# Optimization experiments

Hardware: AMD Instinct MI355X
Metric: run time of the kernel (lower is better)

The kernel has to match this reference:

```python
import jax, jax.numpy as jnp
import numpy as np
import math

D_MODEL = 512
H = 8
DK = D_MODEL // H  # 64
DFF = 2048
EPS = 1e-5


def layernorm(x, g, b):
    mu = jnp.mean(x, axis=-1, keepdims=True)
    var = jnp.mean((x - mu) ** 2, axis=-1, keepdims=True)
    return (x - mu) * jax.lax.rsqrt(var + EPS) * g + b


def gelu(x):
    return jax.nn.gelu(x, approximate=False)  # torch nn.GELU default (erf)


def feedforward(x, W1, b1, lng, lnb, W2, b2):
    x1 = jnp.einsum('btd,df->btf', x, W1) + b1
    x1 = gelu(layernorm(x1, lng, lnb))
    return jnp.einsum('btf,fd->btd', x1, W2) + b2


def setup_inputs() -> dict:
    key = jax.random.key(0)
    ks = iter(jax.random.split(key, 32))
    s = 0.02
    d = {}
    d['x'] = jax.random.normal(next(ks), (4, 2048, D_MODEL), jnp.float32)
    # per-head QKV projections, stacked over heads: [H, d_model, dk]
    d['Wq'] = jax.random.normal(next(ks), (H, D_MODEL, DK), jnp.float32) * s
    d['bq'] = jnp.zeros((H, DK), jnp.float32)
    d['Wk'] = jax.random.normal(next(ks), (H, D_MODEL, DK), jnp.float32) * s
    d['bk'] = jnp.zeros((H, DK), jnp.float32)
    d['Wv'] = jax.random.normal(next(ks), (H, D_MODEL, DK), jnp.float32) * s
    d['bv'] = jnp.zeros((H, DK), jnp.float32)
    d['Wo'] = jax.random.normal(next(ks), (D_MODEL, D_MODEL), jnp.float32) * s
    d['bo'] = jnp.zeros((D_MODEL,), jnp.float32)
    d['ln1_g'] = jnp.ones((D_MODEL,), jnp.float32)
    d['ln1_b'] = jnp.zeros((D_MODEL,), jnp.float32)
    # main FFN
    d['ff_W1'] = jax.random.normal(next(ks), (D_MODEL, DFF), jnp.float32) * s
    d['ff_b1'] = jnp.zeros((DFF,), jnp.float32)
    d['ff_lng'] = jnp.ones((DFF,), jnp.float32)
    d['ff_lnb'] = jnp.zeros((DFF,), jnp.float32)
    d['ff_W2'] = jax.random.normal(next(ks), (DFF, D_MODEL), jnp.float32) * s
    d['ff_b2'] = jnp.zeros((D_MODEL,), jnp.float32)
    d['ln2_g'] = jnp.ones((D_MODEL,), jnp.float32)
    d['ln2_b'] = jnp.zeros((D_MODEL,), jnp.float32)
    d['alphaA'] = jnp.zeros((1,), jnp.float32) + 0.1
    d['alphaB'] = jnp.zeros((1,), jnp.float32) + 0.1
    d['p1'] = jnp.asarray(0.1, jnp.float32)
    # sub1 FFN
    d['s1_W1'] = jax.random.normal(next(ks), (D_MODEL, DFF), jnp.float32) * s
    d['s1_b1'] = jnp.zeros((DFF,), jnp.float32)
    d['s1_lng'] = jnp.ones((DFF,), jnp.float32)
    d['s1_lnb'] = jnp.zeros((DFF,), jnp.float32)
    d['s1_W2'] = jax.random.normal(next(ks), (DFF, D_MODEL), jnp.float32) * s
    d['s1_b2'] = jnp.zeros((D_MODEL,), jnp.float32)
    d['lnsub1_g'] = jnp.ones((D_MODEL,), jnp.float32)
    d['lnsub1_b'] = jnp.zeros((D_MODEL,), jnp.float32)
    d['p2'] = jnp.asarray(0.1, jnp.float32)
    d['sub2_W'] = jax.random.normal(next(ks), (D_MODEL, D_MODEL), jnp.float32) * s
    d['sub2_b'] = jnp.zeros((D_MODEL,), jnp.float32)
    d['lnsub2_g'] = jnp.ones((D_MODEL,), jnp.float32)
    d['lnsub2_b'] = jnp.zeros((D_MODEL,), jnp.float32)
    return d


def reference(x, Wq, bq, Wk, bk, Wv, bv, Wo, bo, ln1_g, ln1_b,
              ff_W1, ff_b1, ff_lng, ff_lnb, ff_W2, ff_b2, ln2_g, ln2_b,
              alphaA, alphaB, p1, s1_W1, s1_b1, s1_lng, s1_lnb, s1_W2, s1_b2,
              lnsub1_g, lnsub1_b, p2, sub2_W, sub2_b, lnsub2_g, lnsub2_b):
    # --- multi-head attention (q = k = v = x) ---
    q = jnp.einsum('btd,hdk->bhtk', x, Wq) + bq[:, None, :]
    k = jnp.einsum('btd,hdk->bhtk', x, Wk) + bk[:, None, :]
    v = jnp.einsum('btd,hdk->bhtk', x, Wv) + bv[:, None, :]
    scores = jnp.einsum('bhtk,bhsk->bhts', q, k) / math.sqrt(DK)
    probs = jax.nn.softmax(scores, axis=-1)
    heads = jnp.einsum('bhts,bhsv->bhtv', probs, v)           # [B,H,T,dv]
    B, _, T, _ = heads.shape
    cat = jnp.transpose(heads, (0, 2, 1, 3)).reshape(B, T, H * DK)
    attn = jnp.einsum('btd,de->bte', cat, Wo) + bo
    # --- residual stack ---
    ln1 = layernorm(x + attn, ln1_g, ln1_b)
    out1 = x + ln1 * alphaA
    fft = feedforward(out1, ff_W1, ff_b1, ff_lng, ff_lnb, ff_W2, ff_b2)
    ln2 = layernorm(fft + out1, ln2_g, ln2_b)
    out2 = out1 + ln2 * alphaB
    # --- sub-branch 1 ---
    sub1 = feedforward(x, s1_W1, s1_b1, s1_lng, s1_lnb, s1_W2, s1_b2)
    sub1 = p1 * gelu(layernorm(sub1, lnsub1_g, lnsub1_b))
    # --- sub-branch 2 ---
    sub2 = jnp.einsum('btd,de->bte', x, sub2_W) + sub2_b
    sub2 = p2 * gelu(layernorm(sub2, lnsub2_g, lnsub2_b))
    return out2 + sub1 + sub2
```

## Files before the change

### kernel.cpp

```cpp
#include <hip/hip_runtime.h>
#include <hip/hip_bf16.h>
#include <math.h>

typedef __hip_bfloat16 bf16;
typedef __attribute__((ext_vector_type(8))) short s8v;
typedef __attribute__((ext_vector_type(4))) float f4v;

#define T_SEQ 2048
#define ROWS 8192
#define DMODEL 512
#define DFF 2048
#define QS 4096

#define GL2LDS(g, l) __builtin_amdgcn_global_load_lds( \
    (const __attribute__((address_space(1))) void*)(g), \
    (__attribute__((address_space(3))) void*)(l), 16, 0, 0)

__device__ __forceinline__ float b2f(bf16 v) { return __bfloat162float(v); }
__device__ __forceinline__ bf16 f2b(float v) { return __float2bfloat16(v); }
__device__ __forceinline__ float us2f(unsigned short u) {
    union { float f; unsigned int u; } c; c.u = ((unsigned int)u) << 16; return c.f;
}
__device__ __forceinline__ unsigned short f2us(float v) {
    bf16 b = f2b(v); return *(unsigned short*)&b;
}
__device__ __forceinline__ float gelu_f(float x) {
    return 0.5f * x * (1.0f + erff(x * 0.70710678118654752440f));
}
__device__ __forceinline__ float ldP(const void* p, int i, bool f32) {
    return f32 ? ((const float*)p)[i] : b2f(((const bf16*)p)[i]);
}

__global__ __launch_bounds__(256) void sniff_kernel(const void* __restrict__ x,
                                                    int* __restrict__ flag) {
    __shared__ float red[4];
    int tid = threadIdx.x;
    const bf16* p = (const bf16*)x;
    float mx = 0.f;
    for (int i = tid; i < 65536; i += 256) {
        float v = b2f(p[i]);
        if (!(v == v)) v = 1e30f;
        mx = fmaxf(mx, fabsf(v));
    }
    #pragma unroll
    for (int o = 32; o; o >>= 1) mx = fmaxf(mx, __shfl_down(mx, o));
    if ((tid & 63) == 0) red[tid >> 6] = mx;
    __syncthreads();
    if (tid == 0) {
        float m = fmaxf(fmaxf(red[0], red[1]), fmaxf(red[2], red[3]));
        flag[0] = (m > 1000.f) ? 1 : 0;
    }
}

__global__ __launch_bounds__(256) void cvt_b16(const void* __restrict__ in,
                                               unsigned short* __restrict__ out, int n,
                                               const int* __restrict__ flag) {
    bool f32 = flag[0] != 0;
    int i = blockIdx.x * 256 + threadIdx.x;
    if (i < n) out[i] = f2us(ldP(in, i, f32));
}

__global__ __launch_bounds__(256) void repack_all(const void* Wq, const void* Wk, const void* Wv,
                                                  const void* s2W, const void* s1W1,
                                                  const void* ffW1, const void* ffW2,
                                                  const void* s1W2, const void* Wo,
                                                  unsigned short* __restrict__ Wbig2,
                                                  unsigned short* __restrict__ ffW1t,
                                                  unsigned short* __restrict__ ffW2t,
                                                  unsigned short* __restrict__ s1W2t,
                                                  unsigned short* __restrict__ Wot,
                                                  const int* __restrict__ flag) {
    bool f32 = flag[0] != 0;
    int idx = blockIdx.x * 256 + threadIdx.x;
    if (idx < 2097152) {
        int n = idx >> 9, d = idx & 511;
        float v;
        if (n < 1536) {
            int sec = n >> 9, nn = n & 511;
            int h = nn >> 6, j = nn & 63;
            const void* W = sec == 0 ? Wq : (sec == 1 ? Wk : Wv);
            v = ldP(W, (h * 512 + d) * 64 + j, f32);
        } else if (n < 2048) {
            v = ldP(s2W, d * 512 + (n - 1536), f32);
        } else {
            v = ldP(s1W1, d * 2048 + (n - 2048), f32);
        }
        Wbig2[idx] = f2us(v);
    } else if (idx < 3145728) {
        int i2 = idx - 2097152;
        int n = i2 >> 9, kd = i2 & 511;
        ffW1t[i2] = f2us(ldP(ffW1, kd * 2048 + n, f32));
    } else if (idx < 4194304) {
        int i2 = idx - 3145728;
        int n = i2 >> 11, kd = i2 & 2047;
        ffW2t[i2] = f2us(ldP(ffW2, kd * 512 + n, f32));
    } else if (idx < 5242880) {
        int i2 = idx - 4194304;
        int n = i2 >> 11, kd = i2 & 2047;
        s1W2t[i2] = f2us(ldP(s1W2, kd * 512 + n, f32));
    } else if (idx < 5505024) {
        int i2 = idx - 5242880;
        int n = i2 >> 9, kd = i2 & 511;
        Wot[i2] = f2us(ldP(Wo, kd * 512 + n, f32));
    }
}

__global__ __launch_bounds__(256) void bias_fuse(const void* bq, const void* bk, const void* bv,
                                                 const void* s2b, const void* s1b1, const void* bo,
                                                 const void* ffb1, const void* ffb2, const void* s1b2,
                                                 float* __restrict__ out,
                                                 const int* __restrict__ flag) {
    bool f32 = flag[0] != 0;
    int i = blockIdx.x * 256 + threadIdx.x;
    if (i >= 7680) return;
    const void* src; int off;
    if      (i < 512)  { src = bq;   off = i; }
    else if (i < 1024) { src = bk;   off = i - 512; }
    else if (i < 1536) { src = bv;   off = i - 1024; }
    else if (i < 2048) { src = s2b;  off = i - 1536; }
    else if (i < 4096) { src = s1b1; off = i - 2048; }
    else if (i < 4608) { src = bo;   off = i - 4096; }
    else if (i < 6656) { src = ffb1; off = i - 4608; }
    else if (i < 7168) { src = ffb2; off = i - 6656; }
    else               { src = s1b2; off = i - 7168; }
    out[i] = ldP(src, off, f32);
}

__global__ __launch_bounds__(256) void gemm_mfma(const unsigned short* __restrict__ A, int lda,
                                                 const unsigned short* __restrict__ Bt,
                                                 const float* __restrict__ bias,
                                                 void* __restrict__ C0,
                                                 void* __restrict__ C1,
                                                 int M, int N, int ldc, int K, int kLen,
                                                 int outBf16) {
    __shared__ unsigned short As[128 * 64];
    __shared__ unsigned short Bs[128 * 64];
    int tid = threadIdx.x;
    int wave = tid >> 6, lane = tid & 63;
    int wm = wave >> 1, wn = wave & 1;
    int quad = lane >> 4, l16 = lane & 15;
    int bm = blockIdx.y * 128, bn = blockIdx.x * 128;
    int z = blockIdx.z;
    int kOff = z * kLen;
    f4v acc[4][4] = {};
    int rsub = lane >> 3;
    int kcst = lane & 7;
    for (int k0 = kOff; k0 < kOff + kLen; k0 += 64) {
        #pragma unroll
        for (int i = 0; i < 4; i++) {
            int rowT = wave * 32 + i * 8 + rsub;
            int kc = (kcst - rowT) & 7;
            GL2LDS(A + (size_t)(bm + rowT) * lda + k0 + kc * 8,
                   &As[(wave * 32 + i * 8) * 64]);
            GL2LDS(Bt + (size_t)(bn + rowT) * K + k0 + kc * 8,
                   &Bs[(wave * 32 + i * 8) * 64]);
        }
        __syncthreads();
        #pragma unroll
        for (int ks = 0; ks < 64; ks += 32) {
            int kchunk = (ks >> 3) + quad;
            s8v af[4], bfr[4];
            #pragma unroll
            for (int mi = 0; mi < 4; mi++) {
                int m = wm * 64 + mi * 16 + l16;
                af[mi] = *(const s8v*)&As[m * 64 + (((kchunk + m) & 7) * 8)];
            }
            #pragma unroll
            for (int ni = 0; ni < 4; ni++) {
                int n = wn * 64 + ni * 16 + l16;
                bfr[ni] = *(const s8v*)&Bs[n * 64 + (((kchunk + n) & 7) * 8)];
            }
            #pragma unroll
            for (int mi = 0; mi < 4; mi++)
                #pragma unroll
                for (int ni = 0; ni < 4; ni++)
                    acc[mi][ni] = __builtin_amdgcn_mfma_f32_16x16x32_bf16(
                        af[mi], bfr[ni], acc[mi][ni], 0, 0, 0);
        }
        __syncthreads();
    }
    bool doBias = (z == 0);
    float bcol[4];
    #pragma unroll
    for (int ni = 0; ni < 4; ni++)
        bcol[ni] = doBias ? bias[bn + wn * 64 + ni * 16 + l16] : 0.f;
    void* Cd = z ? C1 : C0;
    #pragma unroll
    for (int mi = 0; mi < 4; mi++) {
        #pragma unroll
        for (int rg = 0; rg < 4; rg++) {
            size_t row = bm + wm * 64 + mi * 16 + quad * 4 + rg;
            #pragma unroll
            for (int ni = 0; ni < 4; ni++) {
                int col = bn + wn * 64 + ni * 16 + l16;
                float v = acc[mi][ni][rg] + bcol[ni];
                if (outBf16) ((unsigned short*)Cd)[row * ldc + col] = f2us(v);
                else         ((float*)Cd)[row * ldc + col] = v;
            }
        }
    }
}

__global__ __launch_bounds__(256) void transpose_v(const unsigned short* __restrict__ QKV,
                                                   unsigned short* __restrict__ Vt) {
    __shared__ unsigned short tile[64][72];
    int kt = blockIdx.x;
    int bh = blockIdx.y;
    int b = bh >> 3, h = bh & 7;
    const unsigned short* Vg = QKV + ((size_t)b * T_SEQ) * QS + 1024 + h * 64;
    int tid = threadIdx.x;
    int r = tid >> 3, c = (tid & 7) * 8;
    #pragma unroll
    for (int it = 0; it < 2; it++) {
        int rr = r + it * 32;
        uint4 v = *(const uint4*)(Vg + (size_t)(kt * 64 + rr) * QS + c);
        *(uint4*)&tile[rr][c] = v;
    }
    __syncthreads();
    #pragma unroll
    for (int it = 0; it < 2; it++) {
        int d = r + it * 32;
        unsigned short tmp[8];
        #pragma unroll
        for (int j = 0; j < 8; j++) tmp[j] = tile[c + j][d];
        *(uint4*)(Vt + ((size_t)(bh * 64 + d)) * T_SEQ + kt * 64 + c) = *(uint4*)tmp;
    }
}

#define ALD 72
#define SCL2 0.18033688f
__global__ __launch_bounds__(256) void attn_mfma(const unsigned short* __restrict__ QKV,
                                                 const unsigned short* __restrict__ Vt,
                                                 unsigned short* __restrict__ O) {
    __shared__ unsigned short Qs[64 * ALD];
    __shared__ unsigned short Ks[64 * ALD];
    __shared__ unsigned short Vts[64 * ALD];
    __shared__ unsigned short Ps[64 * ALD];

    int tid = threadIdx.x;
    int wave = tid >> 6, lane = tid & 63;
    int quad = lane >> 4, l16 = lane & 15;
    int qbase = blockIdx.x * 64;
    int bh = blockIdx.y;
    int b = bh >> 3, h = bh & 7;
    const unsigned short* Qg = QKV + ((size_t)(b * T_SEQ + qbase)) * QS + h * 64;
    const unsigned short* Kg = QKV + ((size_t)b * T_SEQ) * QS + 512 + h * 64;
    const unsigned short* Vtg = Vt + (size_t)bh * 64 * T_SEQ;

    int r = tid >> 3, c = (tid & 7) * 8;
    #pragma unroll
    for (int it = 0; it < 2; it++) {
        int rr = r + it * 32;
        uint4 v = *(const uint4*)(Qg + (size_t)rr * QS + c);
        *(uint4*)&Qs[rr * ALD + c] = v;
    }
    float lrun[4] = {0.f, 0.f, 0.f, 0.f};
    f4v oacc[4] = {};
    __syncthreads();

    for (int kt = 0; kt < 32; ++kt) {
        #pragma unroll
        for (int it = 0; it < 2; it++) {
            int rr = r + it * 32;
            uint4 kv = *(const uint4*)(Kg + (size_t)(kt * 64 + rr) * QS + c);
            *(uint4*)&Ks[rr * ALD + c] = kv;
            uint4 vv = *(const uint4*)(Vtg + (size_t)rr * T_SEQ + kt * 64 + c);
            *(uint4*)&Vts[rr * ALD + c] = vv;
        }
        __syncthreads();

        f4v sacc[4] = {};
        #pragma unroll
        for (int kc2 = 0; kc2 < 2; kc2++) {
            s8v aq = *(const s8v*)&Qs[(wave * 16 + l16) * ALD + kc2 * 32 + quad * 8];
            #pragma unroll
            for (int ni = 0; ni < 4; ni++) {
                s8v bk_ = *(const s8v*)&Ks[(ni * 16 + l16) * ALD + kc2 * 32 + quad * 8];
                sacc[ni] = __builtin_amdgcn_mfma_f32_16x16x32_bf16(aq, bk_, sacc[ni], 0, 0, 0);
            }
        }
        #pragma unroll
        for (int rg = 0; rg < 4; rg++) {
            #pragma unroll
            for (int ni = 0; ni < 4; ni++) {
                float p = exp2f(fminf(sacc[ni][rg] * SCL2, 30.f));
                lrun[rg] += p;
                Ps[(wave * 16 + quad * 4 + rg) * ALD + ni * 16 + l16] = f2us(p);
            }
        }
        #pragma unroll
        for (int kc2 = 0; kc2 < 2; kc2++) {
            s8v ap = *(const s8v*)&Ps[(wave * 16 + l16) * ALD + kc2 * 32 + quad * 8];
            #pragma unroll
            for (int ni = 0; ni < 4; ni++) {
                s8v bv_ = *(const s8v*)&Vts[(ni * 16 + l16) * ALD + kc2 * 32 + quad * 8];
                oacc[ni] = __builtin_amdgcn_mfma_f32_16x16x32_bf16(ap, bv_, oacc[ni], 0, 0, 0);
            }
        }
        __syncthreads();
    }

    #pragma unroll
    for (int rg = 0; rg < 4; rg++) {
        float l = lrun[rg];
        #pragma unroll
        for (int o = 8; o; o >>= 1) l += __shfl_xor(l, o);
        float linv = 1.0f / l;
        size_t orow = ((size_t)(b * T_SEQ + qbase + wave * 16 + quad * 4 + rg)) * 512 + h * 64;
        #pragma unroll
        for (int ni = 0; ni < 4; ni++)
            O[orow + ni * 16 + l16] = f2us(oacc[ni][rg] * linv);
    }
}

__global__ __launch_bounds__(256) void ln_res1(const void* __restrict__ Xraw,
                                               const unsigned short* __restrict__ Ya,
                                               const unsigned short* __restrict__ Yb,
                                               const void* __restrict__ g,
                                               const void* __restrict__ bb,
                                               const void* __restrict__ alpha,
                                               float* __restrict__ out,
                                               unsigned short* __restrict__ outb,
                                               const int* __restrict__ flag) {
    __shared__ float red[8];
    bool f32 = flag[0] != 0;
    int row = blockIdx.x, tid = threadIdx.x;
    size_t base = (size_t)row * DMODEL;
    float x0 = ldP(Xraw, base + tid, f32);
    float x1 = ldP(Xraw, base + tid + 256, f32);
    float v0 = x0 + us2f(Ya[base + tid]) + us2f(Yb[base + tid]);
    float v1 = x1 + us2f(Ya[base + tid + 256]) + us2f(Yb[base + tid + 256]);
    float s = v0 + v1, s2 = v0 * v0 + v1 * v1;
    #pragma unroll
    for (int o = 32; o; o >>= 1) { s += __shfl_down(s, o); s2 += __shfl_down(s2, o); }
    if ((tid & 63) == 0) { red[tid >> 6] = s; red[4 + (tid >> 6)] = s2; }
    __syncthreads();
    s = red[0] + red[1] + red[2] + red[3];
    s2 = red[4] + red[5] + red[6] + red[7];
    float mu = s * (1.0f / 512.0f);
    float var = s2 * (1.0f / 512.0f) - mu * mu;
    float rr = rsqrtf(var + 1e-5f);
    float a = ldP(alpha, 0, f32);
    float o0 = x0 + a * ((v0 - mu) * rr * ldP(g, tid, f32) + ldP(bb, tid, f32));
    float o1 = x1 + a * ((v1 - mu) * rr * ldP(g, tid + 256, f32) + ldP(bb, tid + 256, f32));
    out[base + tid] = o0;
    out[base + tid + 256] = o1;
    outb[base + tid] = f2us(o0);
    outb[base + tid + 256] = f2us(o1);
}

__global__ __launch_bounds__(256) void ln_res2(const float* __restrict__ Xf,
                                               const float* __restrict__ Y,
                                               const float* __restrict__ Y2,
                                               const void* __restrict__ g,
                                               const void* __restrict__ bb,
                                               const void* __restrict__ alpha,
                                               float* __restrict__ out,
                                               const int* __restrict__ flag) {
    __shared__ float red[8];
    bool f32 = flag[0] != 0;
    int row = blockIdx.x, tid = threadIdx.x;
    size_t base = (size_t)row * DMODEL;
    float x0 = Xf[base + tid], x1 = Xf[base + tid + 256];
    float v0 = x0 + Y[base + tid] + Y2[base + tid];
    float v1 = x1 + Y[base + tid + 256] + Y2[base + tid + 256];
    float s = v0 + v1, s2 = v0 * v0 + v1 * v1;
    #pragma unroll
    for (int o = 32; o; o >>= 1) { s += __shfl_down(s, o); s2 += __shfl_down(s2, o); }
    if ((tid & 63) == 0) { red[tid >> 6] = s; red[4 + (tid >> 6)] = s2; }
    __syncthreads();
    s = red[0] + red[1] + red[2] + red[3];
    s2 = red[4] + red[5] + red[6] + red[7];
    float mu = s * (1.0f / 512.0f);
    float var = s2 * (1.0f / 512.0f) - mu * mu;
    float rr = rsqrtf(var + 1e-5f);
    float a = ldP(alpha, 0, f32);
    out[base + tid] = x0 + a * ((v0 - mu) * rr * ldP(g, tid, f32) + ldP(bb, tid, f32));
    out[base + tid + 256] = x1 + a * ((v1 - mu) * rr * ldP(g, tid + 256, f32) + ldP(bb, tid + 256, f32));
}

__global__ __launch_bounds__(256) void ln_gelu(unsigned short* __restrict__ Hm, int stride,
                                               const void* __restrict__ g,
                                               const void* __restrict__ bb,
                                               const int* __restrict__ flag) {
    __shared__ float red[8];
    bool f32 = flag[0] != 0;
    int row = blockIdx.x, tid = threadIdx.x;
    size_t base = (size_t)row * stride;
    float v[8];
    float s = 0.f, s2 = 0.f;
    #pragma unroll
    for (int i = 0; i < 8; i++) {
        v[i] = us2f(Hm[base + tid + i * 256]);
        s += v[i]; s2 += v[i] * v[i];
    }
    #pragma unroll
    for (int o = 32; o; o >>= 1) { s += __shfl_down(s, o); s2 += __shfl_down(s2, o); }
    if ((tid & 63) == 0) { red[tid >> 6] = s; red[4 + (tid >> 6)] = s2; }
    __syncthreads();
    s = red[0] + red[1] + red[2] + red[3];
    s2 = red[4] + red[5] + red[6] + red[7];
    float mu = s * (1.0f / 2048.0f);
    float var = s2 * (1.0f / 2048.0f) - mu * mu;
    float r = rsqrtf(var + 1e-5f);
    #pragma unroll
    for (int i = 0; i < 8; i++) {
        int cc = tid + i * 256;
        float ln = (v[i] - mu) * r * ldP(g, cc, f32) + ldP(bb, cc, f32);
        Hm[base + cc] = f2us(gelu_f(ln));
    }
}

__global__ __launch_bounds__(256) void final_kernel(const float* __restrict__ O2,
                                                    const unsigned short* __restrict__ S1,
                                                    const unsigned short* __restrict__ S1b,
                                                    const unsigned short* __restrict__ S2,
                                                    const void* __restrict__ g1,
                                                    const void* __restrict__ b1,
                                                    const void* __restrict__ g2,
                                                    const void* __restrict__ b2,
                                                    const void* __restrict__ p1,
                                                    const void* __restrict__ p2,
                                                    void* __restrict__ out,
                                                    const int* __restrict__ flag) {
    __shared__ float red[16];
    bool f32 = flag[0] != 0;
    int row = blockIdx.x, tid = threadIdx.x;
    size_t base = (size_t)row * DMODEL;
    size_t base2 = (size_t)row * QS;
    float a0 = us2f(S1[base + tid]) + us2f(S1b[base + tid]);
    float a1 = us2f(S1[base + tid + 256]) + us2f(S1b[base + tid + 256]);
    float c0 = us2f(S2[base2 + tid]);
    float c1 = us2f(S2[base2 + tid + 256]);
    float sa = a0 + a1, sa2 = a0 * a0 + a1 * a1;
    float sc = c0 + c1, sc2 = c0 * c0 + c1 * c1;
    #pragma unroll
    for (int o = 32; o; o >>= 1) {
        sa += __shfl_down(sa, o); sa2 += __shfl_down(sa2, o);
        sc += __shfl_down(sc, o); sc2 += __shfl_down(sc2, o);
    }
    int w = tid >> 6;
    if ((tid & 63) == 0) { red[w] = sa; red[4 + w] = sa2; red[8 + w] = sc; red[12 + w] = sc2; }
    __syncthreads();
    sa = red[0] + red[1] + red[2] + red[3];
    sa2 = red[4] + red[5] + red[6] + red[7];
    sc = red[8] + red[9] + red[10] + red[11];
    sc2 = red[12] + red[13] + red[14] + red[15];
    float mua = sa * (1.0f / 512.0f), vara = sa2 * (1.0f / 512.0f) - mua * mua;
    float ra = rsqrtf(vara + 1e-5f);
    float muc = sc * (1.0f / 512.0f), varc = sc2 * (1.0f / 512.0f) - muc * muc;
    float rc = rsqrtf(varc + 1e-5f);
    float fp1 = ldP(p1, 0, f32), fp2 = ldP(p2, 0, f32);
    float av[2] = {a0, a1}, cv[2] = {c0, c1};
    #pragma unroll
    for (int i = 0; i < 2; i++) {
        int cc = tid + i * 256;
        float l1 = (av[i] - mua) * ra * ldP(g1, cc, f32) + ldP(b1, cc, f32);
        float l2 = (cv[i] - muc) * rc * ldP(g2, cc, f32) + ldP(b2, cc, f32);
        float o = O2[base + cc] + fp1 * gelu_f(l1) + fp2 * gelu_f(l2);
        if (f32) ((float*)out)[base + cc] = o;
        else     ((bf16*)out)[base + cc] = f2b(o);
    }
}

extern "C" void kernel_launch(void* const* d_in, const int* in_sizes, int n_in,
                              void* d_out, int out_size, void* d_ws, size_t ws_size,
                              hipStream_t stream) {
    (void)in_sizes; (void)n_in; (void)out_size; (void)ws_size;
    const void* x      = d_in[0];
    const void* Wq     = d_in[1];
    const void* bq     = d_in[2];
    const void* Wk     = d_in[3];
    const void* bk     = d_in[4];
    const void* Wv     = d_in[5];
    const void* bv     = d_in[6];
    const void* Wo     = d_in[7];
    const void* bo     = d_in[8];
    const void* ln1_g  = d_in[9];
    const void* ln1_b  = d_in[10];
    const void* ffW1   = d_in[11];
    const void* ffb1   = d_in[12];
    const void* fflng  = d_in[13];
    const void* fflnb  = d_in[14];
    const void* ffW2   = d_in[15];
    const void* ffb2   = d_in[16];
    const void* ln2_g  = d_in[17];
    const void* ln2_b  = d_in[18];
    const void* alphaA = d_in[19];
    const void* alphaB = d_in[20];
    const void* p1     = d_in[21];
    const void* s1W1   = d_in[22];
    const void* s1b1   = d_in[23];
    const void* s1lng  = d_in[24];
    const void* s1lnb  = d_in[25];
    const void* s1W2   = d_in[26];
    const void* s1b2   = d_in[27];
    const void* lns1g  = d_in[28];
    const void* lns1b  = d_in[29];
    const void* p2     = d_in[30];
    const void* s2W    = d_in[31];
    const void* s2b    = d_in[32];
    const void* lns2g  = d_in[33];
    const void* lns2b  = d_in[34];

    char* base = (char*)d_ws;
    size_t off = 0;
    auto alloc = [&](size_t bytes) {
        char* p = base + off;
        off += (bytes + 255) & ~(size_t)255;
        return p;
    };
    int* flag             = (int*)alloc(256);
    unsigned short* Wbig2 = (unsigned short*)alloc((size_t)4096 * 512 * 2);
    unsigned short* ffW1t = (unsigned short*)alloc((size_t)2048 * 512 * 2);
    unsigned short* ffW2t = (unsigned short*)alloc((size_t)512 * 2048 * 2);
    unsigned short* s1W2t = (unsigned short*)alloc((size_t)512 * 2048 * 2);
    unsigned short* Wot   = (unsigned short*)alloc(512 * 512 * 2);
    float* bias_all       = (float*)alloc(7680 * 4);
    char*  regX           = alloc((size_t)ROWS * 512 * 2);
    char*  regCat         = alloc((size_t)ROWS * 512 * 2);
    unsigned short* Cbig2 = (unsigned short*)alloc((size_t)ROWS * QS * 2);
    char*  regB           = alloc((size_t)ROWS * 512 * 2);
    char*  regD           = alloc((size_t)ROWS * 512 * 2);
    float* out1           = (float*)alloc((size_t)ROWS * 512 * 4);
    char*  regO           = alloc((size_t)ROWS * 512 * 4);

    unsigned short* xb    = (unsigned short*)regX;
    unsigned short* Vtb   = (unsigned short*)regX;
    unsigned short* out1b = (unsigned short*)regX;
    unsigned short* catb  = (unsigned short*)regCat;
    float* fft            = (float*)regX;
    unsigned short* sub1raw  = (unsigned short*)regB;
    unsigned short* sub1raw2 = (unsigned short*)regD;
    unsigned short* attnA = (unsigned short*)regO;
    unsigned short* attnB = (unsigned short*)(regO + (size_t)ROWS * 512 * 2);
    float* fft2           = (float*)regO;
    float* out2           = (float*)regO;

    float* biasBig = bias_all + 0;
    float* biasWo  = bias_all + 4096;
    float* biasF1  = bias_all + 4608;
    float* biasF2  = bias_all + 6656;
    float* biasS12 = bias_all + 7168;

    sniff_kernel<<<1, 256, 0, stream>>>(x, flag);
    cvt_b16<<<(ROWS * 512 + 255) / 256, 256, 0, stream>>>(x, xb, ROWS * 512, flag);
    repack_all<<<(5505024 + 255) / 256, 256, 0, stream>>>(
        Wq, Wk, Wv, s2W, s1W1, ffW1, ffW2, s1W2, Wo,
        Wbig2, ffW1t, ffW2t, s1W2t, Wot, flag);
    bias_fuse<<<30, 256, 0, stream>>>(bq, bk, bv, s2b, s1b1, bo, ffb1, ffb2, s1b2,
                                      bias_all, flag);

    auto gemm = [&](const unsigned short* A, int lda, const unsigned short* Bt,
                    const float* bias, void* C0, void* C1,
                    int M, int N, int ldc, int K, int outBf16, int split) {
        int kLen = split ? K / 2 : K;
        gemm_mfma<<<dim3(N / 128, M / 128, split ? 2 : 1), 256, 0, stream>>>(
            A, lda, Bt, bias, C0, C1, M, N, ldc, K, kLen, outBf16);
    };

    gemm(xb, 512, Wbig2, biasBig, Cbig2, nullptr, ROWS, 4096, 4096, 512, 1, 0);
    transpose_v<<<dim3(32, 32), 256, 0, stream>>>(Cbig2, Vtb);
    attn_mfma<<<dim3(T_SEQ / 64, 32), 256, 0, stream>>>(Cbig2, Vtb, catb);
    ln_gelu<<<ROWS, 256, 0, stream>>>(Cbig2 + 2048, QS, s1lng, s1lnb, flag);
    gemm(Cbig2 + 2048, QS, s1W2t, biasS12, sub1raw, sub1raw2, ROWS, 512, 512, 2048, 1, 1);
    gemm(catb, 512, Wot, biasWo, attnA, attnB, ROWS, 512, 512, 512, 1, 1);
    ln_res1<<<ROWS, 256, 0, stream>>>(x, attnA, attnB, ln1_g, ln1_b, alphaA,
                                      out1, out1b, flag);
    gemm(out1b, 512, ffW1t, biasF1, Cbig2 + 2048, nullptr, ROWS, 2048, 4096, 512, 1, 0);
    ln_gelu<<<ROWS, 256, 0, stream>>>(Cbig2 + 2048, QS, fflng, fflnb, flag);
    gemm(Cbig2 + 2048, QS, ffW2t, biasF2, fft, fft2, ROWS, 512, 512, 2048, 0, 1);
    ln_res2<<<ROWS, 256, 0, stream>>>(out1, fft, fft2, ln2_g, ln2_b, alphaB, out2, flag);
    final_kernel<<<ROWS, 256, 0, stream>>>(out2, sub1raw, sub1raw2, Cbig2 + 1536,
                                           lns1g, lns1b, lns2g, lns2b,
                                           p1, p2, d_out, flag);
}
```

Before: 558.8 us.

## Fuse prep kernels, V transpose into QKV GEMM, paired GEMMs, and final LN

Merges the dtype sniff, input conversion, weight repack and bias gather into one prep kernel, where each block detects the input dtype from the first 256 elements. The QKV GEMM epilogue now writes the transposed V directly, removing the separate transpose kernel. The sub1 second-layer GEMM and the Wo GEMM run in one paired launch, and ln_res2 is folded into the final kernel. Together these cut launch count and intermediate traffic. The cost is a strided scalar transposed store in the GEMM epilogue and a weaker dtype sniff that samples fewer elements.

```diff
diff --git a/kernel.cpp b/kernel.cpp
--- a/kernel.cpp
+++ b/kernel.cpp
@@ -31,99 +31,168 @@
     return f32 ? ((const float*)p)[i] : b2f(((const bf16*)p)[i]);
 }
 
-__global__ __launch_bounds__(256) void sniff_kernel(const void* __restrict__ x,
-                                                    int* __restrict__ flag) {
+#define XB_E 4194304
+#define RP_E 5505024
+__global__ __launch_bounds__(256) void prep_all(
+    const void* __restrict__ x,
+    const void* Wq, const void* Wk, const void* Wv, const void* s2W,
+    const void* s1W1, const void* ffW1, const void* ffW2, const void* s1W2,
+    const void* Wo,
+    const void* bq, const void* bk, const void* bv, const void* s2b,
+    const void* s1b1, const void* bo, const void* ffb1, const void* ffb2,
+    const void* s1b2,
+    unsigned short* __restrict__ xb, unsigned short* __restrict__ Wbig2,
+    unsigned short* __restrict__ ffW1t, unsigned short* __restrict__ ffW2t,
+    unsigned short* __restrict__ s1W2t, unsigned short* __restrict__ Wot,
+    float* __restrict__ bias_all, int* __restrict__ flag)
+{
     __shared__ float red[4];
+    __shared__ int lf;
     int tid = threadIdx.x;
-    const bf16* p = (const bf16*)x;
-    float mx = 0.f;
-    for (int i = tid; i < 65536; i += 256) {
-        float v = b2f(p[i]);
+    {
+        float v = b2f(((const bf16*)x)[tid]);
         if (!(v == v)) v = 1e30f;
-        mx = fmaxf(mx, fabsf(v));
-    }
-    #pragma unroll
-    for (int o = 32; o; o >>= 1) mx = fmaxf(mx, __shfl_down(mx, o));
-    if ((tid & 63) == 0) red[tid >> 6] = mx;
-    __syncthreads();
-    if (tid == 0) {
-        float m = fmaxf(fmaxf(red[0], red[1]), fmaxf(red[2], red[3]));
-        flag[0] = (m > 1000.f) ? 1 : 0;
-    }
-}
-
-__global__ __launch_bounds__(256) void cvt_b16(const void* __restrict__ in,
-                                               unsigned short* __restrict__ out, int n,
-                                               const int* __restrict__ flag) {
-    bool f32 = flag[0] != 0;
-    int i = blockIdx.x * 256 + threadIdx.x;
-    if (i < n) out[i] = f2us(ldP(in, i, f32));
-}
-
-__global__ __launch_bounds__(256) void repack_all(const void* Wq, const void* Wk, const void* Wv,
-                                                  const void* s2W, const void* s1W1,
-                                                  const void* ffW1, const void* ffW2,
-                                                  const void* s1W2, const void* Wo,
-                                                  unsigned short* __restrict__ Wbig2,
-                                                  unsigned short* __restrict__ ffW1t,
-                                                  unsigned short* __restrict__ ffW2t,
-                                                  unsigned short* __restrict__ s1W2t,
-                                                  unsigned short* __restrict__ Wot,
-                                                  const int* __restrict__ flag) {
-    bool f32 = flag[0] != 0;
-    int idx = blockIdx.x * 256 + threadIdx.x;
-    if (idx < 2097152) {
-        int n = idx >> 9, d = idx & 511;
-        float v;
-        if (n < 1536) {
-            int sec = n >> 9, nn = n & 511;
-            int h = nn >> 6, j = nn & 63;
-            const void* W = sec == 0 ? Wq : (sec == 1 ? Wk : Wv);
-            v = ldP(W, (h * 512 + d) * 64 + j, f32);
-        } else if (n < 2048) {
-            v = ldP(s2W, d * 512 + (n - 1536), f32);
+        float mx = fabsf(v);
+        #pragma unroll
+        for (int o = 32; o; o >>= 1) mx = fmaxf(mx, __shfl_down(mx, o));
+        if ((tid & 63) == 0) red[tid >> 6] = mx;
+        __syncthreads();
+        if (tid == 0)
+            lf = (fmaxf(fmaxf(red[0], red[1]), fmaxf(red[2], red[3])) > 1000.f) ? 1 : 0;
+        __syncthreads();
+    }
+    bool f32 = lf != 0;
+    if (blockIdx.x == 0 && tid == 0) flag[0] = lf;
+
+    int idx = blockIdx.x * 256 + tid;
+    if (idx < XB_E) {
+        xb[idx] = f2us(ldP(x, idx, f32));
+        return;
+    }
+    idx -= XB_E;
+    if (idx < RP_E) {
+        if (idx < 2097152) {
+            int n = idx >> 9, d = idx & 511;
+            float v;
+            if (n < 1536) {
+                int sec = n >> 9, nn = n & 511;
+                int h = nn >> 6, j = nn & 63;
+                const void* W = sec == 0 ? Wq : (sec == 1 ? Wk : Wv);
+                v = ldP(W, (h * 512 + d) * 64 + j, f32);
+            } else if (n < 2048) {
+                v = ldP(s2W, d * 512 + (n - 1536), f32);
+            } else {
+                v = ldP(s1W1, d * 2048 + (n - 2048), f32);
+            }
+            Wbig2[idx] = f2us(v);
+        } else if (idx < 3145728) {
+            int i2 = idx - 2097152;
+            int n = i2 >> 9, kd = i2 & 511;
+            ffW1t[i2] = f2us(ldP(ffW1, kd * 2048 + n, f32));
+        } else if (idx < 4194304) {
+            int i2 = idx - 3145728;
+            int n = i2 >> 11, kd = i2 & 2047;
+            ffW2t[i2] = f2us(ldP(ffW2, kd * 512 + n, f32));
+        } else if (idx < 5242880) {
+            int i2 = idx - 4194304;
+            int n = i2 >> 11, kd = i2 & 2047;
+            s1W2t[i2] = f2us(ldP(s1W2, kd * 512 + n, f32));
         } else {
-            v = ldP(s1W1, d * 2048 + (n - 2048), f32);
-        }
-        Wbig2[idx] = f2us(v);
-    } else if (idx < 3145728) {
-        int i2 = idx - 2097152;
-        int n = i2 >> 9, kd = i2 & 511;
-        ffW1t[i2] = f2us(ldP(ffW1, kd * 2048 + n, f32));
-    } else if (idx < 4194304) {
-        int i2 = idx - 3145728;
-        int n = i2 >> 11, kd = i2 & 2047;
-        ffW2t[i2] = f2us(ldP(ffW2, kd * 512 + n, f32));
-    } else if (idx < 5242880) {
-        int i2 = idx - 4194304;
-        int n = i2 >> 11, kd = i2 & 2047;
-        s1W2t[i2] = f2us(ldP(s1W2, kd * 512 + n, f32));
-    } else if (idx < 5505024) {
-        int i2 = idx - 5242880;
-        int n = i2 >> 9, kd = i2 & 511;
-        Wot[i2] = f2us(ldP(Wo, kd * 512 + n, f32));
-    }
-}
-
-__global__ __launch_bounds__(256) void bias_fuse(const void* bq, const void* bk, const void* bv,
-                                                 const void* s2b, const void* s1b1, const void* bo,
-                                                 const void* ffb1, const void* ffb2, const void* s1b2,
-                                                 float* __restrict__ out,
-                                                 const int* __restrict__ flag) {
-    bool f32 = flag[0] != 0;
-    int i = blockIdx.x * 256 + threadIdx.x;
-    if (i >= 7680) return;
-    const void* src; int off;
-    if      (i < 512)  { src = bq;   off = i; }
-    else if (i < 1024) { src = bk;   off = i - 512; }
-    else if (i < 1536) { src = bv;   off = i - 1024; }
-    else if (i < 2048) { src = s2b;  off = i - 1536; }
-    else if (i < 4096) { src = s1b1; off = i - 2048; }
-    else if (i < 4608) { src = bo;   off = i - 4096; }
-    else if (i < 6656) { src = ffb1; off = i - 4608; }
-    else if (i < 7168) { src = ffb2; off = i - 6656; }
-    else               { src = s1b2; off = i - 7168; }
-    out[i] = ldP(src, off, f32);
+            int i2 = idx - 5242880;
+            int n = i2 >> 9, kd = i2 & 511;
+            Wot[i2] = f2us(ldP(Wo, kd * 512 + n, f32));
+        }
+        return;
+    }
+    idx -= RP_E;
+    if (idx < 7680) {
+        const void* src; int off;
+        if      (idx < 512)  { src = bq;   off = idx; }
+        else if (idx < 1024) { src = bk;   off = idx - 512; }
+        else if (idx < 1536) { src = bv;   off = idx - 1024; }
+        else if (idx < 2048) { src = s2b;  off = idx - 1536; }
+        else if (idx < 4096) { src = s1b1; off = idx - 2048; }
+        else if (idx < 4608) { src = bo;   off = idx - 4096; }
+        else if (idx < 6656) { src = ffb1; off = idx - 4608; }
+        else if (idx < 7168) { src = ffb2; off = idx - 6656; }
+        else                 { src = s1b2; off = idx - 7168; }
+        bias_all[idx] = ldP(src, off, f32);
+    }
+}
+
+__device__ __forceinline__ void gemm_core(
+    unsigned short* __restrict__ As, unsigned short* __restrict__ Bs,
+    const unsigned short* __restrict__ A, int lda,
+    const unsigned short* __restrict__ Bt,
+    const float* __restrict__ bias,
+    void* __restrict__ Cd, int ldc, int Kst,
+    int kOff, int kLen, int doBias, int outBf16, int bm, int bn,
+    unsigned short* __restrict__ Vt)
+{
+    int tid = threadIdx.x;
+    int wave = tid >> 6, lane = tid & 63;
+    int wm = wave >> 1, wn = wave & 1;
+    int quad = lane >> 4, l16 = lane & 15;
+    f4v acc[4][4] = {};
+    int rsub = lane >> 3;
+    int kcst = lane & 7;
+    for (int k0 = kOff; k0 < kOff + kLen; k0 += 64) {
+        #pragma unroll
+        for (int i = 0; i < 4; i++) {
+            int rowT = wave * 32 + i * 8 + rsub;
+            int kc = (kcst - rowT) & 7;
+            GL2LDS(A + (size_t)(bm + rowT) * lda + k0 + kc * 8,
+                   &As[(wave * 32 + i * 8) * 64]);
+            GL2LDS(Bt + (size_t)(bn + rowT) * Kst + k0 + kc * 8,
+                   &Bs[(wave * 32 + i * 8) * 64]);
+        }
+        __syncthreads();
+        #pragma unroll
+        for (int ks = 0; ks < 64; ks += 32) {
+            int kchunk = (ks >> 3) + quad;
+            s8v af[4], bfr[4];
+            #pragma unroll
+            for (int mi = 0; mi < 4; mi++) {
+                int m = wm * 64 + mi * 16 + l16;
+                af[mi] = *(const s8v*)&As[m * 64 + (((kchunk + m) & 7) * 8)];
+            }
+            #pragma unroll
+            for (int ni = 0; ni < 4; ni++) {
+                int n = wn * 64 + ni * 16 + l16;
+                bfr[ni] = *(const s8v*)&Bs[n * 64 + (((kchunk + n) & 7) * 8)];
+            }
+            #pragma unroll
+            for (int mi = 0; mi < 4; mi++)
+                #pragma unroll
+                for (int ni = 0; ni < 4; ni++)
+                    acc[mi][ni] = __builtin_amdgcn_mfma_f32_16x16x32_bf16(
+                        af[mi], bfr[ni], acc[mi][ni], 0, 0, 0);
+        }
+        __syncthreads();
+    }
+    float bcol[4];
+    #pragma unroll
+    for (int ni = 0; ni < 4; ni++)
+        bcol[ni] = doBias ? bias[bn + wn * 64 + ni * 16 + l16] : 0.f;
+    #pragma unroll
+    for (int mi = 0; mi < 4; mi++) {
+        #pragma unroll
+        for (int rg = 0; rg < 4; rg++) {
+            size_t row = bm + wm * 64 + mi * 16 + quad * 4 + rg;
+            #pragma unroll
+            for (int ni = 0; ni < 4; ni++) {
+                int col = bn + wn * 64 + ni * 16 + l16;
+                float v = acc[mi][ni][rg] + bcol[ni];
+                if (outBf16) ((unsigned short*)Cd)[row * ldc + col] = f2us(v);
+                else         ((float*)Cd)[row * ldc + col] = v;
+                if (Vt && col >= 1024 && col < 1536) {
+                    int hd = col - 1024;
+                    int b = (int)(row >> 11), t = (int)(row & 2047);
+                    Vt[((size_t)b * 512 + hd) * 2048 + t] = f2us(v);
+                }
+            }
+        }
+    }
 }
 
 __global__ __launch_bounds__(256) void gemm_mfma(const unsigned short* __restrict__ A, int lda,
@@ -131,99 +200,34 @@
                                                  const float* __restrict__ bias,
                                                  void* __restrict__ C0,
                                                  void* __restrict__ C1,
-                                                 int M, int N, int ldc, int K, int kLen,
-                                                 int outBf16) {
+                                                 int ldc, int K, int kLen, int outBf16,
+                                                 unsigned short* __restrict__ Vt) {
     __shared__ unsigned short As[128 * 64];
     __shared__ unsigned short Bs[128 * 64];
-    int tid = threadIdx.x;
-    int wave = tid >> 6, lane = tid & 63;
-    int wm = wave >> 1, wn = wave & 1;
-    int quad = lane >> 4, l16 = lane & 15;
-    int bm = blockIdx.y * 128, bn = blockIdx.x * 128;
     int z = blockIdx.z;
-    int kOff = z * kLen;
-    f4v acc[4][4] = {};
-    int rsub = lane >> 3;
-    int kcst = lane & 7;
-    for (int k0 = kOff; k0 < kOff + kLen; k0 += 64) {
-        #pragma unroll
-        for (int i = 0; i < 4; i++) {
-            int rowT = wave * 32 + i * 8 + rsub;
-            int kc = (kcst - rowT) & 7;
-            GL2LDS(A + (size_t)(bm + rowT) * lda + k0 + kc * 8,
-                   &As[(wave * 32 + i * 8) * 64]);
-            GL2LDS(Bt + (size_t)(bn + rowT) * K + k0 + kc * 8,
-                   &Bs[(wave * 32 + i * 8) * 64]);
-        }
-        __syncthreads();
-        #pragma unroll
-        for (int ks = 0; ks < 64; ks += 32) {
-            int kchunk = (ks >> 3) + quad;
-            s8v af[4], bfr[4];
-            #pragma unroll
-            for (int mi = 0; mi < 4; mi++) {
-                int m = wm * 64 + mi * 16 + l16;
-                af[mi] = *(const s8v*)&As[m * 64 + (((kchunk + m) & 7) * 8)];
-            }
-            #pragma unroll
-            for (int ni = 0; ni < 4; ni++) {
-                int n = wn * 64 + ni * 16 + l16;
-                bfr[ni] = *(const s8v*)&Bs[n * 64 + (((kchunk + n) & 7) * 8)];
-            }
-            #pragma unroll
-            for (int mi = 0; mi < 4; mi++)
-                #pragma unroll
-                for (int ni = 0; ni < 4; ni++)
-                    acc[mi][ni] = __builtin_amdgcn_mfma_f32_16x16x32_bf16(
-                        af[mi], bfr[ni], acc[mi][ni], 0, 0, 0);
-        }
-        __syncthreads();
-    }
-    bool doBias = (z == 0);
-    float bcol[4];
-    #pragma unroll
-    for (int ni = 0; ni < 4; ni++)
-        bcol[ni] = doBias ? bias[bn + wn * 64 + ni * 16 + l16] : 0.f;
-    void* Cd = z ? C1 : C0;
-    #pragma unroll
-    for (int mi = 0; mi < 4; mi++) {
-        #pragma unroll
-        for (int rg = 0; rg < 4; rg++) {
-            size_t row = bm + wm * 64 + mi * 16 + quad * 4 + rg;
-            #pragma unroll
-            for (int ni = 0; ni < 4; ni++) {
-                int col = bn + wn * 64 + ni * 16 + l16;
-                float v = acc[mi][ni][rg] + bcol[ni];
-                if (outBf16) ((unsigned short*)Cd)[row * ldc + col] = f2us(v);
-                else         ((float*)Cd)[row * ldc + col] = v;
-            }
-        }
-    }
-}
-
-__global__ __launch_bounds__(256) void transpose_v(const unsigned short* __restrict__ QKV,
-                                                   unsigned short* __restrict__ Vt) {
-    __shared__ unsigned short tile[64][72];
-    int kt = blockIdx.x;
-    int bh = blockIdx.y;
-    int b = bh >> 3, h = bh & 7;
-    const unsigned short* Vg = QKV + ((size_t)b * T_SEQ) * QS + 1024 + h * 64;
-    int tid = threadIdx.x;
-    int r = tid >> 3, c = (tid & 7) * 8;
-    #pragma unroll
-    for (int it = 0; it < 2; it++) {
-        int rr = r + it * 32;
-        uint4 v = *(const uint4*)(Vg + (size_t)(kt * 64 + rr) * QS + c);
-        *(uint4*)&tile[rr][c] = v;
-    }
-    __syncthreads();
-    #pragma unroll
-    for (int it = 0; it < 2; it++) {
-        int d = r + it * 32;
-        unsigned short tmp[8];
-        #pragma unroll
-        for (int j = 0; j < 8; j++) tmp[j] = tile[c + j][d];
-        *(uint4*)(Vt + ((size_t)(bh * 64 + d)) * T_SEQ + kt * 64 + c) = *(uint4*)tmp;
+    gemm_core(As, Bs, A, lda, Bt, bias, z ? C1 : C0, ldc, K,
+              z * kLen, kLen, z == 0, outBf16,
+              blockIdx.y * 128, blockIdx.x * 128, Vt);
+}
+
+__global__ __launch_bounds__(256) void gemm_pair(
+    const unsigned short* __restrict__ A1, int lda1,
+    const unsigned short* __restrict__ Bt1, const float* __restrict__ bias1,
+    void* __restrict__ C1a, void* __restrict__ C1b, int K1,
+    const unsigned short* __restrict__ A2, int lda2,
+    const unsigned short* __restrict__ Bt2, const float* __restrict__ bias2,
+    void* __restrict__ C2a, void* __restrict__ C2b, int K2) {
+    __shared__ unsigned short As[128 * 64];
+    __shared__ unsigned short Bs[128 * 64];
+    int z = blockIdx.z;
+    if (z < 2) {
+        int kLen = K1 / 2;
+        gemm_core(As, Bs, A1, lda1, Bt1, bias1, z ? C1b : C1a, 512, K1,
+                  z * kLen, kLen, z == 0, 1, blockIdx.y * 128, blockIdx.x * 128, nullptr);
+    } else {
+        int zz = z - 2, kLen = K2 / 2;
+        gemm_core(As, Bs, A2, lda2, Bt2, bias2, zz ? C2b : C2a, 512, K2,
+                  zz * kLen, kLen, zz == 0, 1, blockIdx.y * 128, blockIdx.x * 128, nullptr);
     }
 }
 
@@ -349,36 +353,6 @@
     outb[base + tid + 256] = f2us(o1);
 }
 
-__global__ __launch_bounds__(256) void ln_res2(const float* __restrict__ Xf,
-                                               const float* __restrict__ Y,
-                                               const float* __restrict__ Y2,
-                                               const void* __restrict__ g,
-                                               const void* __restrict__ bb,
-                                               const void* __restrict__ alpha,
-                                               float* __restrict__ out,
-                                               const int* __restrict__ flag) {
-    __shared__ float red[8];
-    bool f32 = flag[0] != 0;
-    int row = blockIdx.x, tid = threadIdx.x;
-    size_t base = (size_t)row * DMODEL;
-    float x0 = Xf[base + tid], x1 = Xf[base + tid + 256];
-    float v0 = x0 + Y[base + tid] + Y2[base + tid];
-    float v1 = x1 + Y[base + tid + 256] + Y2[base + tid + 256];
-    float s = v0 + v1, s2 = v0 * v0 + v1 * v1;
-    #pragma unroll
-    for (int o = 32; o; o >>= 1) { s += __shfl_down(s, o); s2 += __shfl_down(s2, o); }
-    if ((tid & 63) == 0) { red[tid >> 6] = s; red[4 + (tid >> 6)] = s2; }
-    __syncthreads();
-    s = red[0] + red[1] + red[2] + red[3];
-    s2 = red[4] + red[5] + red[6] + red[7];
-    float mu = s * (1.0f / 512.0f);
-    float var = s2 * (1.0f / 512.0f) - mu * mu;
-    float rr = rsqrtf(var + 1e-5f);
-    float a = ldP(alpha, 0, f32);
-    out[base + tid] = x0 + a * ((v0 - mu) * rr * ldP(g, tid, f32) + ldP(bb, tid, f32));
-    out[base + tid + 256] = x1 + a * ((v1 - mu) * rr * ldP(g, tid + 256, f32) + ldP(bb, tid + 256, f32));
-}
-
 __global__ __launch_bounds__(256) void ln_gelu(unsigned short* __restrict__ Hm, int stride,
                                                const void* __restrict__ g,
                                                const void* __restrict__ bb,
@@ -411,53 +385,72 @@
     }
 }
 
-__global__ __launch_bounds__(256) void final_kernel(const float* __restrict__ O2,
-                                                    const unsigned short* __restrict__ S1,
-                                                    const unsigned short* __restrict__ S1b,
-                                                    const unsigned short* __restrict__ S2,
-                                                    const void* __restrict__ g1,
-                                                    const void* __restrict__ b1,
-                                                    const void* __restrict__ g2,
-                                                    const void* __restrict__ b2,
-                                                    const void* __restrict__ p1,
-                                                    const void* __restrict__ p2,
-                                                    void* __restrict__ out,
-                                                    const int* __restrict__ flag) {
-    __shared__ float red[16];
+__global__ __launch_bounds__(256) void final2(const float* __restrict__ out1,
+                                              const float* __restrict__ fft,
+                                              const float* __restrict__ fft2,
+                                              const unsigned short* __restrict__ S1,
+                                              const unsigned short* __restrict__ S1b,
+                                              const unsigned short* __restrict__ S2,
+                                              const void* __restrict__ g2ln,
+                                              const void* __restrict__ b2ln,
+                                              const void* __restrict__ alphaB,
+                                              const void* __restrict__ g1s,
+                                              const void* __restrict__ b1s,
+                                              const void* __restrict__ g2s,
+                                              const void* __restrict__ b2s,
+                                              const void* __restrict__ p1,
+                                              const void* __restrict__ p2,
+                                              void* __restrict__ out,
+                                              const int* __restrict__ flag) {
+    __shared__ float red[24];
     bool f32 = flag[0] != 0;
     int row = blockIdx.x, tid = threadIdx.x;
     size_t base = (size_t)row * DMODEL;
     size_t base2 = (size_t)row * QS;
+    float x0 = out1[base + tid], x1 = out1[base + tid + 256];
+    float v0 = x0 + fft[base + tid] + fft2[base + tid];
+    float v1 = x1 + fft[base + tid + 256] + fft2[base + tid + 256];
     float a0 = us2f(S1[base + tid]) + us2f(S1b[base + tid]);
     float a1 = us2f(S1[base + tid + 256]) + us2f(S1b[base + tid + 256]);
     float c0 = us2f(S2[base2 + tid]);
     float c1 = us2f(S2[base2 + tid + 256]);
+    float sv = v0 + v1, sv2 = v0 * v0 + v1 * v1;
     float sa = a0 + a1, sa2 = a0 * a0 + a1 * a1;
     float sc = c0 + c1, sc2 = c0 * c0 + c1 * c1;
     #pragma unroll
     for (int o = 32; o; o >>= 1) {
+        sv += __shfl_down(sv, o); sv2 += __shfl_down(sv2, o);
         sa += __shfl_down(sa, o); sa2 += __shfl_down(sa2, o);
         sc += __shfl_down(sc, o); sc2 += __shfl_down(sc2, o);
     }
     int w = tid >> 6;
-    if ((tid & 63) == 0) { red[w] = sa; red[4 + w] = sa2; red[8 + w] = sc; red[12 + w] = sc2; }
+    if ((tid & 63) == 0) {
+        red[w] = sv; red[4 + w] = sv2; red[8 + w] = sa;
+        red[12 + w] = sa2; red[16 + w] = sc; red[20 + w] = sc2;
+    }
     __syncthreads();
-    sa = red[0] + red[1] + red[2] + red[3];
-    sa2 = red[4] + red[5] + red[6] + red[7];
-    sc = red[8] + red[9] + red[10] + red[11];
-    sc2 = red[12] + red[13] + red[14] + red[15];
+    sv = red[0] + red[1] + red[2] + red[3];
+    sv2 = red[4] + red[5] + red[6] + red[7];
+    sa = red[8] + red[9] + red[10] + red[11];
+    sa2 = red[12] + red[13] + red[14] + red[15];
+    sc = red[16] + red[17] + red[18] + red[19];
+    sc2 = red[20] + red[21] + red[22] + red[23];
+    float muv = sv * (1.0f / 512.0f), varv = sv2 * (1.0f / 512.0f) - muv * muv;
+    float rv = rsqrtf(varv + 1e-5f);
     float mua = sa * (1.0f / 512.0f), vara = sa2 * (1.0f / 512.0f) - mua * mua;
     float ra = rsqrtf(vara + 1e-5f);
     float muc = sc * (1.0f / 512.0f), varc = sc2 * (1.0f / 512.0f) - muc * muc;
     float rc = rsqrtf(varc + 1e-5f);
+    float aB = ldP(alphaB, 0, f32);
     float fp1 = ldP(p1, 0, f32), fp2 = ldP(p2, 0, f32);
-    float av[2] = {a0, a1}, cv[2] = {c0, c1};
+    float xv[2] = {x0, x1}, vv[2] = {v0, v1}, av[2] = {a0, a1}, cv[2] = {c0, c1};
     #pragma unroll
     for (int i = 0; i < 2; i++) {
         int cc = tid + i * 256;
-        float l1 = (av[i] - mua) * ra * ldP(g1, cc, f32) + ldP(b1, cc, f32);
-        float l2 = (cv[i] - muc) * rc * ldP(g2, cc, f32) + ldP(b2, cc, f32);
-        float o = O2[base + cc] + fp1 * gelu_f(l1) + fp2 * gelu_f(l2);
+        float out2 = xv[i] + aB * ((vv[i] - muv) * rv * ldP(g2ln, cc, f32) + ldP(b2ln, cc, f32));
+        float l1 = (av[i] - mua) * ra * ldP(g1s, cc, f32) + ldP(b1s, cc, f32);
+        float l2 = (cv[i] - muc) * rc * ldP(g2s, cc, f32) + ldP(b2s, cc, f32);
+        float o = out2 + fp1 * gelu_f(l1) + fp2 * gelu_f(l2);
         if (f32) ((float*)out)[base + cc] = o;
         else     ((bf16*)out)[base + cc] = f2b(o);
     }
@@ -526,16 +519,15 @@
     char*  regO           = alloc((size_t)ROWS * 512 * 4);
 
     unsigned short* xb    = (unsigned short*)regX;
-    unsigned short* Vtb   = (unsigned short*)regX;
     unsigned short* out1b = (unsigned short*)regX;
     unsigned short* catb  = (unsigned short*)regCat;
     float* fft            = (float*)regX;
     unsigned short* sub1raw  = (unsigned short*)regB;
     unsigned short* sub1raw2 = (unsigned short*)regD;
+    unsigned short* Vtb   = (unsigned short*)regO;
     unsigned short* attnA = (unsigned short*)regO;
     unsigned short* attnB = (unsigned short*)(regO + (size_t)ROWS * 512 * 2);
     float* fft2           = (float*)regO;
-    float* out2           = (float*)regO;
 
     float* biasBig = bias_all + 0;
     float* biasWo  = bias_all + 4096;
@@ -543,35 +535,35 @@
     float* biasF2  = bias_all + 6656;
     float* biasS12 = bias_all + 7168;
 
-    sniff_kernel<<<1, 256, 0, stream>>>(x, flag);
-    cvt_b16<<<(ROWS * 512 + 255) / 256, 256, 0, stream>>>(x, xb, ROWS * 512, flag);
-    repack_all<<<(5505024 + 255) / 256, 256, 0, stream>>>(
-        Wq, Wk, Wv, s2W, s1W1, ffW1, ffW2, s1W2, Wo,
-        Wbig2, ffW1t, ffW2t, s1W2t, Wot, flag);
-    bias_fuse<<<30, 256, 0, stream>>>(bq, bk, bv, s2b, s1b1, bo, ffb1, ffb2, s1b2,
-                                      bias_all, flag);
-
-    auto gemm = [&](const unsigned short* A, int lda, const unsigned short* Bt,
-                    const float* bias, void* C0, void* C1,
-                    int M, int N, int ldc, int K, int outBf16, int split) {
-        int kLen = split ? K / 2 : K;
-        gemm_mfma<<<dim3(N / 128, M / 128, split ? 2 : 1), 256, 0, stream>>>(
-            A, lda, Bt, bias, C0, C1, M, N, ldc, K, kLen, outBf16);
-    };
-
-    gemm(xb, 512, Wbig2, biasBig, Cbig2, nullptr, ROWS, 4096, 4096, 512, 1, 0);
-    transpose_v<<<dim3(32, 32), 256, 0, stream>>>(Cbig2, Vtb);
+    prep_all<<<(XB_E + RP_E + 7680) / 256, 256, 0, stream>>>(
+        x, Wq, Wk, Wv, s2W, s1W1, ffW1, ffW2, s1W2, Wo,
+        bq, bk, bv, s2b, s1b1, bo, ffb1, ffb2, s1b2,
+        xb, Wbig2, ffW1t, ffW2t, s1W2t, Wot, bias_all, flag);
+
+    gemm_mfma<<<dim3(32, 64, 1), 256, 0, stream>>>(
+        xb, 512, Wbig2, biasBig, Cbig2, nullptr, 4096, 512, 512, 1, Vtb);
+
     attn_mfma<<<dim3(T_SEQ / 64, 32), 256, 0, stream>>>(Cbig2, Vtb, catb);
+
     ln_gelu<<<ROWS, 256, 0, stream>>>(Cbig2 + 2048, QS, s1lng, s1lnb, flag);
-    gemm(Cbig2 + 2048, QS, s1W2t, biasS12, sub1raw, sub1raw2, ROWS, 512, 512, 2048, 1, 1);
-    gemm(catb, 512, Wot, biasWo, attnA, attnB, ROWS, 512, 512, 512, 1, 1);
+
+    gemm_pair<<<dim3(4, 64, 4), 256, 0, stream>>>(
+        Cbig2 + 2048, QS, s1W2t, biasS12, sub1raw, sub1raw2, 2048,
+        catb, 512, Wot, biasWo, attnA, attnB, 512);
+
     ln_res1<<<ROWS, 256, 0, stream>>>(x, attnA, attnB, ln1_g, ln1_b, alphaA,
                                       out1, out1b, flag);
-    gemm(out1b, 512, ffW1t, biasF1, Cbig2 + 2048, nullptr, ROWS, 2048, 4096, 512, 1, 0);
+
+    gemm_mfma<<<dim3(16, 64, 1), 256, 0, stream>>>(
+        out1b, 512, ffW1t, biasF1, Cbig2 + 2048, nullptr, 4096, 512, 512, 1, nullptr);
+
     ln_gelu<<<ROWS, 256, 0, stream>>>(Cbig2 + 2048, QS, fflng, fflnb, flag);
-    gemm(Cbig2 + 2048, QS, ffW2t, biasF2, fft, fft2, ROWS, 512, 512, 2048, 0, 1);
-    ln_res2<<<ROWS, 256, 0, stream>>>(out1, fft, fft2, ln2_g, ln2_b, alphaB, out2, flag);
-    final_kernel<<<ROWS, 256, 0, stream>>>(out2, sub1raw, sub1raw2, Cbig2 + 1536,
-                                           lns1g, lns1b, lns2g, lns2b,
-                                           p1, p2, d_out, flag);
-}
+
+    gemm_mfma<<<dim3(4, 64, 2), 256, 0, stream>>>(
+        Cbig2 + 2048, QS, ffW2t, biasF2, fft, fft2, 512, 2048, 1024, 0, nullptr);
+
+    final2<<<ROWS, 256, 0, stream>>>(out1, fft, fft2, sub1raw, sub1raw2, Cbig2 + 1536,
+                                     ln2_g, ln2_b, alphaB,
+                                     lns1g, lns1b, lns2g, lns2b,
+                                     p1, p2, d_out, flag);
+}
```

Result: faster. 511.1 us (-8.5%).
